# Performance work log

Hardware: AMD Instinct MI355X
Metric: run time of the kernel (lower is better)

Reference implementation:

```python
import jax, jax.numpy as jnp
import numpy as np
from jax import lax

STRIDE = 1
PAD = 1
KH = KW = 3


def conv2d(x, w, b=None, stride=STRIDE, pad=PAD):
    out = lax.conv_general_dilated(x, w, (stride, stride), [(pad, pad), (pad, pad)],
                                   dimension_numbers=("NCHW", "OIHW", "NCHW"))
    if b is not None:
        out = out + b[None, :, None, None]
    return out


def deform_conv2d(x, offset, mask, weight, stride=STRIDE, pad=PAD):
    """torchvision.ops.deform_conv2d (v2, single group) semantics."""
    B, C, H, W = x.shape
    Co, Ci, Kh, Kw = weight.shape
    K2 = Kh * Kw
    Ho = (H + 2 * pad - Kh) // stride + 1
    Wo = (W + 2 * pad - Kw) // stride + 1

    off = offset.reshape(B, K2, 2, Ho, Wo)  # [...,0]=dy, [...,1]=dx (row-major kernel order)
    ky = (jnp.arange(K2) // Kw).astype(x.dtype)
    kx = (jnp.arange(K2) % Kw).astype(x.dtype)
    hs = (jnp.arange(Ho) * stride - pad).astype(x.dtype)
    ws = (jnp.arange(Wo) * stride - pad).astype(x.dtype)

    # sampling coords [B, K2, Ho, Wo]
    py = off[:, :, 0] + hs[None, None, :, None] + ky[None, :, None, None]
    px = off[:, :, 1] + ws[None, None, None, :] + kx[None, :, None, None]

    y0 = jnp.floor(py)
    x0 = jnp.floor(px)
    wy1 = py - y0
    wx1 = px - x0
    wy0 = 1.0 - wy1
    wx0 = 1.0 - wx1
    y0i = y0.astype(jnp.int32)
    x0i = x0.astype(jnp.int32)

    xf = x.reshape(B, C, H * W)

    def gather(yi, xi):
        valid = (yi >= 0) & (yi < H) & (xi >= 0) & (xi < W)
        lin = jnp.clip(yi, 0, H - 1) * W + jnp.clip(xi, 0, W - 1)  # [B,K2,Ho,Wo]
        linf = lin.reshape(B, 1, -1)
        g = jnp.take_along_axis(xf, jnp.broadcast_to(linf, (B, C, linf.shape[-1])), axis=2)
        g = g.reshape(B, C, K2, Ho, Wo)
        return g * valid[:, None].astype(x.dtype)

    # bilinear combine, modulated by mask; v: [B, C, K2, Ho, Wo]
    v = ((wy0 * wx0)[:, None] * gather(y0i, x0i)
         + (wy0 * wx1)[:, None] * gather(y0i, x0i + 1)
         + (wy1 * wx0)[:, None] * gather(y0i + 1, x0i)
         + (wy1 * wx1)[:, None] * gather(y0i + 1, x0i + 1))
    v = v * mask[:, None]

    return jnp.einsum('bckhw,ock->bohw', v, weight.reshape(Co, Ci, K2))


def setup_inputs() -> dict:
    key = jax.random.key(0)
    ks = jax.random.split(key, 6)
    B, C, H, W = 2, 256, 64, 64
    Co = 256
    fan = C * KH * KW
    return {
        "x": jax.random.normal(ks[0], (B, C, H, W), jnp.float32),
        "residual": jax.random.normal(ks[1], (B, C, H, W), jnp.float32),
        "offset_w": jax.random.normal(ks[2], (2 * KH * KW, C, KH, KW), jnp.float32) * np.sqrt(2.0 / fan),
        "offset_b": jnp.zeros((2 * KH * KW,), jnp.float32),
        "mod_w": jax.random.normal(ks[3], (KH * KW, C, KH, KW), jnp.float32) * np.sqrt(2.0 / fan),
        "mod_b": jnp.zeros((KH * KW,), jnp.float32),
        "reg_w": jax.random.normal(ks[4], (Co, C, KH, KW), jnp.float32) * np.sqrt(2.0 / fan),
    }


def reference(x, residual, offset_w, offset_b, mod_w, mod_b, reg_w):
    offset = conv2d(residual, offset_w, offset_b)
    modulator = 2.0 * jax.nn.sigmoid(conv2d(x, mod_w, mod_b))
    return deform_conv2d(x, offset, modulator, reg_w)
```

## Files before the change

### kernel.cpp

```cpp
#include <hip/hip_runtime.h>
#include <hip/hip_bf16.h>
#include <math.h>

#define BB 2
#define CC 256
#define HH 64
#define WW 64
#define COo 256
#define HWs 4096
#define K2 9
#define CK 2304

typedef __attribute__((ext_vector_type(4))) float floatx4;
typedef __attribute__((ext_vector_type(8))) short shortx8;

#define O_OFF   0
#define O_MASK  147456
#define O_WBF   221184
#define O_WPK   516096
#define O_XT    10027008
#define O_RT    11075584

__device__ __forceinline__ void gll16(const __hip_bfloat16* g, __hip_bfloat16* l) {
    __builtin_amdgcn_global_load_lds(
        (const __attribute__((address_space(1))) unsigned int*)g,
        (__attribute__((address_space(3))) unsigned int*)l, 16, 0, 0);
}

__device__ __forceinline__ short f2bf(float v) {
    __hip_bfloat16 h = __float2bfloat16(v);
    return *reinterpret_cast<short*>(&h);
}

__device__ __forceinline__ float bf2f(short s) {
    unsigned u = ((unsigned)(unsigned short)s) << 16;
    return __builtin_bit_cast(float, u);
}

__global__ __launch_bounds__(256) void prep_kernel(
    const float* __restrict__ x,
    const float* __restrict__ residual,
    const float* __restrict__ reg_w,
    const float* __restrict__ off_w,
    const float* __restrict__ mod_w,
    __hip_bfloat16* __restrict__ xT,
    __hip_bfloat16* __restrict__ resT,
    __hip_bfloat16* __restrict__ Wbf,
    __hip_bfloat16* __restrict__ Wpk)
{
    int blk = blockIdx.x;
    int t = threadIdx.x;
    if (blk < 2048) {
        int sel = blk >> 10;
        int bk  = blk & 1023;
        int oc = bk & 7;
        int y  = (bk >> 3) & 63;
        int b  = bk >> 9;
        int wo = t & 63;
        int cg = t >> 6;
        int c0 = oc * 32 + cg * 8;
        const float* src = (sel ? residual : x)
                           + ((size_t)(b * CC + c0) * HH + y) * WW + wo;
        shortx8 pk;
#pragma unroll
        for (int j = 0; j < 8; ++j) pk[j] = f2bf(src[(size_t)j * HWs]);
        __hip_bfloat16* dst = sel ? resT : xT;
        *(shortx8*)(dst + ((size_t)b * 4096 + y * 64 + wo) * 256 + c0) = pk;
    } else {
        int idx = (blk - 2048) * 256 + t;
        if (idx < CK * COo) {
            int co = idx / CK;
            int r  = idx - co * CK;
            int k  = r >> 8;
            int c  = r & 255;
            Wbf[idx] = __float2bfloat16(reg_w[(size_t)co * CK + c * 9 + k]);
        }
        if (idx < 147456) {
            int g    = idx / 73728;
            int rem  = idx % 73728;
            int kc   = rem / 9216;
            int r2   = rem % 9216;
            int tap  = r2 / 1024;
            int r3   = r2 & 1023;
            int nf   = r3 >> 9;
            int r4   = r3 & 511;
            int lane = r4 >> 3;
            int j    = r4 & 7;
            int c    = kc * 32 + (lane >> 4) * 8 + j;
            int n    = nf * 16 + (lane & 15);
            float v = 0.f;
            if (g == 0) { if (n < 18) v = off_w[((size_t)n * CC + c) * 9 + tap]; }
            else        { if (n < 9)  v = mod_w[((size_t)n * CC + c) * 9 + tap]; }
            Wpk[idx] = __float2bfloat16(v);
        }
    }
}

__global__ __launch_bounds__(512) void convA2_kernel(
    const __hip_bfloat16* __restrict__ xT,
    const __hip_bfloat16* __restrict__ resT,
    const __hip_bfloat16* __restrict__ Wpk,
    const float* __restrict__ off_b,
    const float* __restrict__ mod_b,
    float* __restrict__ off_out,
    float* __restrict__ mask_out)
{
    int blk = blockIdx.x;
    int tile = blk & 127;
    int g = (blk >> 7) & 1;
    int b = blk >> 8;
    int t = threadIdx.x;
    int lane = t & 63;
    int w = t >> 6;
    int ph = w & 1;
    int ks = w >> 1;
    int ln = lane & 15;
    int quad = lane >> 4;

    const __hip_bfloat16* src = (g ? xT : resT) + (size_t)b * 4096 * 256;
    const __hip_bfloat16* wg  = Wpk + (size_t)g * 73728 + (size_t)ks * 2 * 9216;

    int pix = tile * 32 + ph * 16 + ln;
    int ho = pix >> 6, wo = pix & 63;

    floatx4 acc0 = (floatx4){0.f, 0.f, 0.f, 0.f};
    floatx4 acc1 = (floatx4){0.f, 0.f, 0.f, 0.f};

#pragma unroll
    for (int tap = 0; tap < 9; ++tap) {
        int ky = tap / 3, kx = tap % 3;
        int r  = ho + ky - 1;
        int cx = wo + kx - 1;
        bool v = (r >= 0) && (r < HH) && (cx >= 0) && (cx < WW);
        int hw = v ? (r * WW + cx) : 0;
        const __hip_bfloat16* abase = src + (size_t)hw * 256 + quad * 8 + ks * 64;
        const __hip_bfloat16* wbase = wg + (size_t)tap * 1024 + lane * 8;
#pragma unroll
        for (int kc = 0; kc < 2; ++kc) {
            shortx8 af = *(const shortx8*)(abase + kc * 32);
            if (!v) {
                shortx8 zf = {0,0,0,0,0,0,0,0};
                af = zf;
            }
            shortx8 b0 = *(const shortx8*)(wbase + (size_t)kc * 9216);
            shortx8 b1 = *(const shortx8*)(wbase + (size_t)kc * 9216 + 512);
            acc0 = __builtin_amdgcn_mfma_f32_16x16x32_bf16(af, b0, acc0, 0, 0, 0);
            acc1 = __builtin_amdgcn_mfma_f32_16x16x32_bf16(af, b1, acc1, 0, 0, 0);
        }
    }

    __shared__ float s_red[8][64][8];
    *(floatx4*)&s_red[w][lane][0] = acc0;
    *(floatx4*)&s_red[w][lane][4] = acc1;
    __syncthreads();
    if (w < 2) {
#pragma unroll
        for (int j = 0; j < 4; ++j) {
            acc0[j] = s_red[w][lane][j]     + s_red[w + 2][lane][j]
                    + s_red[w + 4][lane][j] + s_red[w + 6][lane][j];
            acc1[j] = s_red[w][lane][4 + j]     + s_red[w + 2][lane][4 + j]
                    + s_red[w + 4][lane][4 + j] + s_red[w + 6][lane][4 + j];
        }

#pragma unroll
        for (int nf = 0; nf < 2; ++nf) {
            floatx4 a = nf ? acc1 : acc0;
            int n = nf * 16 + ln;
#pragma unroll
            for (int i2 = 0; i2 < 4; ++i2) {
                int p = tile * 32 + w * 16 + quad * 4 + i2;
                if (g == 0) {
                    if (n < 18)
                        off_out[((size_t)b * 18 + n) * HWs + p] = a[i2] + off_b[n];
                } else {
                    if (n < 9) {
                        float z = a[i2] + mod_b[n];
                        mask_out[((size_t)b * 9 + n) * HWs + p] =
                            2.f / (1.f + __expf(-z));
                    }
                }
            }
        }
    }
}

__global__ __launch_bounds__(256) void gemm_fused_kernel(
    const __hip_bfloat16* __restrict__ xT,
    const float* __restrict__ off,
    const float* __restrict__ mask,
    const __hip_bfloat16* __restrict__ Wbf,
    float* __restrict__ out)
{
    int blk0 = blockIdx.x;
    int blk = ((blk0 & 7) << 6) | (blk0 >> 3);
    int nt = blk & 1;
    int mt = blk >> 1;
    int t  = threadIdx.x;
    int lane = t & 63;
    int w    = t >> 6;
    int quad = lane >> 4;
    int ln   = lane & 15;
    int wm = w & 1;
    int wn = w >> 1;

    __shared__ __hip_bfloat16 As[2][32 * 64];
    __shared__ __hip_bfloat16 Bs[2][128 * 64];
    __shared__ int   s_mi[32][K2][4];
    __shared__ float s_mw[32][K2][4];
    __shared__ float s_out[4][16 * 20];

    int b = mt >> 7;
    const __hip_bfloat16* xb = xT + (size_t)b * 4096 * 256;

    int lr8 = lane >> 3;
    int sub = lane & 7;
    int chk = sub ^ lr8;

    const __hip_bfloat16* gB = Wbf + (size_t)(nt * 128 + w * 8 + lr8) * CK + chk * 8;
    int lof = w * 512;

    floatx4 acc[4];
#pragma unroll
    for (int nf = 0; nf < 4; ++nf) acc[nf] = (floatx4){0.f, 0.f, 0.f, 0.f};

#pragma unroll
    for (int h = 0; h < 4; ++h)
        gll16(gB + (size_t)(h * 32) * CK, &Bs[0][lof + h * 2048]);

    for (int u = t; u < 32 * K2; u += 256) {
        int pl_ = u / K2;
        int k  = u - pl_ * K2;
        int pix = mt * 32 + pl_;
        int hw = pix & 4095;
        int ho = hw >> 6, wo = hw & 63;
        float dy = off [(((size_t)b * 18 + 2 * k    ) << 12) + hw];
        float dx = off [(((size_t)b * 18 + 2 * k + 1) << 12) + hw];
        float m  = mask[(((size_t)b * 9  + k        ) << 12) + hw];
        float py = (float)(ho - 1 + k / 3) + dy;
        float px = (float)(wo - 1 + k % 3) + dx;
        float y0f = floorf(py), x0f = floorf(px);
        float wy1 = py - y0f, wx1 = px - x0f;
        float wy0 = 1.f - wy1, wx0 = 1.f - wx1;
        int y0 = (int)y0f, x0 = (int)x0f;
#pragma unroll
        for (int j = 0; j < 4; ++j) {
            int yy = y0 + (j >> 1);
            int xx = x0 + (j & 1);
            float wj = ((j == 0) ? wy0 * wx0 :
                        (j == 1) ? wy0 * wx1 :
                        (j == 2) ? wy1 * wx0 : wy1 * wx1) * m;
            bool valid = (yy >= 0) && (yy < HH) && (xx >= 0) && (xx < WW);
            s_mi[pl_][k][j] = valid ? (yy * WW + xx) : 0;
            s_mw[pl_][k][j] = valid ? wj : 0.f;
        }
    }

    int pl  = t >> 3;
    int ch8 = t & 7;
    int aslot = pl * 64 + ((ch8 ^ (pl & 7)) * 8);

    int   mi0, mi1, mi2, mi3;
    float mw0, mw1, mw2, mw3;
    auto meta_load = [&](int k) {
        mi0 = s_mi[pl][k][0]; mi1 = s_mi[pl][k][1];
        mi2 = s_mi[pl][k][2]; mi3 = s_mi[pl][k][3];
        mw0 = s_mw[pl][k][0]; mw1 = s_mw[pl][k][1];
        mw2 = s_mw[pl][k][2]; mw3 = s_mw[pl][k][3];
    };

    shortx8 gc0, gc1, gc2, gc3;
    float   gw0, gw1, gw2, gw3;
    auto gather_load = [&](int cb) {
        const __hip_bfloat16* xr = xb + cb * 64 + ch8 * 8;
        gc0 = *(const shortx8*)(xr + (size_t)mi0 * 256);
        gc1 = *(const shortx8*)(xr + (size_t)mi1 * 256);
        gc2 = *(const shortx8*)(xr + (size_t)mi2 * 256);
        gc3 = *(const shortx8*)(xr + (size_t)mi3 * 256);
        gw0 = mw0; gw1 = mw1; gw2 = mw2; gw3 = mw3;
    };
    auto gather_store = [&](int buf) {
        shortx8 o;
#pragma unroll
        for (int j = 0; j < 8; ++j)
            o[j] = f2bf(gw0 * bf2f(gc0[j]) + gw1 * bf2f(gc1[j])
                      + gw2 * bf2f(gc2[j]) + gw3 * bf2f(gc3[j]));
        *(shortx8*)&As[buf][aslot] = o;
    };

    __syncthreads();
    meta_load(0);
    gather_load(0);
    gather_store(0);
    gather_load(1);

    int swz = ln & 7;

    for (int kt = 0; kt < 36; ++kt) {
        int cur = kt & 1;
        int nxt = cur ^ 1;
        __syncthreads();
        if (kt + 1 < 36) {
            int ko = (kt + 1) * 64;
#pragma unroll
            for (int h = 0; h < 4; ++h)
                gll16(gB + (size_t)(h * 32) * CK + ko, &Bs[nxt][lof + h * 2048]);
        }
#pragma unroll
        for (int kh = 0; kh < 2; ++kh) {
            int slot = ((kh * 4 + quad) ^ swz) * 8;
            shortx8 af = *(const shortx8*)
                &As[cur][(wm * 16 + ln) * 64 + slot];
            shortx8 bf[4];
#pragma unroll
            for (int nf = 0; nf < 4; ++nf)
                bf[nf] = *(const shortx8*)
                    &Bs[cur][(wn * 64 + nf * 16 + ln) * 64 + slot];
#pragma unroll
            for (int nf = 0; nf < 4; ++nf)
                acc[nf] = __builtin_amdgcn_mfma_f32_16x16x32_bf16(
                    af, bf[nf], acc[nf], 0, 0, 0);
        }
        if (kt + 1 < 36) gather_store(nxt);
        if (kt + 2 < 36) {
            int k2 = kt + 2;
            if ((k2 & 3) == 0) meta_load(k2 >> 2);
            gather_load(k2 & 3);
        }
    }

    int bb = mt >> 7;
    int hw0 = (mt & 127) * 32 + wm * 16;
    float* sw = &s_out[w][0];
    int co_l = lane >> 2;
    int seg  = lane & 3;
#pragma unroll
    for (int nf = 0; nf < 4; ++nf) {
        *(floatx4*)&sw[ln * 20 + quad * 4] = acc[nf];
        floatx4 v0 = *(const floatx4*)&sw[co_l * 20 + seg * 4];
        int co = nt * 128 + wn * 64 + nf * 16 + co_l;
        float* orow = out + ((size_t)(bb * COo + co) << 12) + hw0;
        *(floatx4*)&orow[seg * 4] = v0;
    }
}

extern "C" void kernel_launch(void* const* d_in, const int* in_sizes, int n_in,
                              void* d_out, int out_size, void* d_ws, size_t ws_size,
                              hipStream_t stream)
{
    const float* x     = (const float*)d_in[0];
    const float* resid = (const float*)d_in[1];
    const float* off_w = (const float*)d_in[2];
    const float* off_b = (const float*)d_in[3];
    const float* mod_w = (const float*)d_in[4];
    const float* mod_b = (const float*)d_in[5];
    const float* reg_w = (const float*)d_in[6];
    float* out = (float*)d_out;

    float* ws = (float*)d_ws;
    float* off_buf   = ws + O_OFF;
    float* mask_buf  = ws + O_MASK;
    __hip_bfloat16* Wbf  = (__hip_bfloat16*)(ws + O_WBF);
    __hip_bfloat16* Wpk  = (__hip_bfloat16*)(ws + O_WPK);
    __hip_bfloat16* xT   = (__hip_bfloat16*)(ws + O_XT);
    __hip_bfloat16* resT = (__hip_bfloat16*)(ws + O_RT);

    prep_kernel<<<2048 + (CK * COo + 255) / 256, 256, 0, stream>>>(
        x, resid, reg_w, off_w, mod_w, xT, resT, Wbf, Wpk);

    convA2_kernel<<<512, 512, 0, stream>>>(xT, resT, Wpk, off_b, mod_b,
                                           off_buf, mask_buf);

    gemm_fused_kernel<<<512, 256, 0, stream>>>(xT, off_buf, mask_buf, Wbf, out);
}
```

Baseline: 130.6 us.

## Fuse offset/mask convolution into deformable GEMM kernel via shared memory

Merges the offset and modulator 3x3 convolutions into the main deformable-conv GEMM kernel. Each block computes the offsets and masks for its 32 pixels with MFMA and keeps them in shared memory instead of writing them to and reading them from global buffers. This removes one kernel launch and the global round-trip. In exchange, both N-tile blocks recompute the same conv, and the per-block conv runs without split-K before the main loop, adding serial latency.

```diff
diff --git a/kernel.cpp b/kernel.cpp
--- a/kernel.cpp
+++ b/kernel.cpp
@@ -14,8 +14,6 @@
 typedef __attribute__((ext_vector_type(4))) float floatx4;
 typedef __attribute__((ext_vector_type(8))) short shortx8;
 
-#define O_OFF   0
-#define O_MASK  147456
 #define O_WBF   221184
 #define O_WPK   516096
 #define O_XT    10027008
@@ -96,98 +94,12 @@
     }
 }
 
-__global__ __launch_bounds__(512) void convA2_kernel(
+__global__ __launch_bounds__(256) void mega_kernel(
     const __hip_bfloat16* __restrict__ xT,
     const __hip_bfloat16* __restrict__ resT,
     const __hip_bfloat16* __restrict__ Wpk,
     const float* __restrict__ off_b,
     const float* __restrict__ mod_b,
-    float* __restrict__ off_out,
-    float* __restrict__ mask_out)
-{
-    int blk = blockIdx.x;
-    int tile = blk & 127;
-    int g = (blk >> 7) & 1;
-    int b = blk >> 8;
-    int t = threadIdx.x;
-    int lane = t & 63;
-    int w = t >> 6;
-    int ph = w & 1;
-    int ks = w >> 1;
-    int ln = lane & 15;
-    int quad = lane >> 4;
-
-    const __hip_bfloat16* src = (g ? xT : resT) + (size_t)b * 4096 * 256;
-    const __hip_bfloat16* wg  = Wpk + (size_t)g * 73728 + (size_t)ks * 2 * 9216;
-
-    int pix = tile * 32 + ph * 16 + ln;
-    int ho = pix >> 6, wo = pix & 63;
-
-    floatx4 acc0 = (floatx4){0.f, 0.f, 0.f, 0.f};
-    floatx4 acc1 = (floatx4){0.f, 0.f, 0.f, 0.f};
-
-#pragma unroll
-    for (int tap = 0; tap < 9; ++tap) {
-        int ky = tap / 3, kx = tap % 3;
-        int r  = ho + ky - 1;
-        int cx = wo + kx - 1;
-        bool v = (r >= 0) && (r < HH) && (cx >= 0) && (cx < WW);
-        int hw = v ? (r * WW + cx) : 0;
-        const __hip_bfloat16* abase = src + (size_t)hw * 256 + quad * 8 + ks * 64;
-        const __hip_bfloat16* wbase = wg + (size_t)tap * 1024 + lane * 8;
-#pragma unroll
-        for (int kc = 0; kc < 2; ++kc) {
-            shortx8 af = *(const shortx8*)(abase + kc * 32);
-            if (!v) {
-                shortx8 zf = {0,0,0,0,0,0,0,0};
-                af = zf;
-            }
-            shortx8 b0 = *(const shortx8*)(wbase + (size_t)kc * 9216);
-            shortx8 b1 = *(const shortx8*)(wbase + (size_t)kc * 9216 + 512);
-            acc0 = __builtin_amdgcn_mfma_f32_16x16x32_bf16(af, b0, acc0, 0, 0, 0);
-            acc1 = __builtin_amdgcn_mfma_f32_16x16x32_bf16(af, b1, acc1, 0, 0, 0);
-        }
-    }
-
-    __shared__ float s_red[8][64][8];
-    *(floatx4*)&s_red[w][lane][0] = acc0;
-    *(floatx4*)&s_red[w][lane][4] = acc1;
-    __syncthreads();
-    if (w < 2) {
-#pragma unroll
-        for (int j = 0; j < 4; ++j) {
-            acc0[j] = s_red[w][lane][j]     + s_red[w + 2][lane][j]
-                    + s_red[w + 4][lane][j] + s_red[w + 6][lane][j];
-            acc1[j] = s_red[w][lane][4 + j]     + s_red[w + 2][lane][4 + j]
-                    + s_red[w + 4][lane][4 + j] + s_red[w + 6][lane][4 + j];
-        }
-
-#pragma unroll
-        for (int nf = 0; nf < 2; ++nf) {
-            floatx4 a = nf ? acc1 : acc0;
-            int n = nf * 16 + ln;
-#pragma unroll
-            for (int i2 = 0; i2 < 4; ++i2) {
-                int p = tile * 32 + w * 16 + quad * 4 + i2;
-                if (g == 0) {
-                    if (n < 18)
-                        off_out[((size_t)b * 18 + n) * HWs + p] = a[i2] + off_b[n];
-                } else {
-                    if (n < 9) {
-                        float z = a[i2] + mod_b[n];
-                        mask_out[((size_t)b * 9 + n) * HWs + p] =
-                            2.f / (1.f + __expf(-z));
-                    }
-                }
-            }
-        }
-    }
-}
-
-__global__ __launch_bounds__(256) void gemm_fused_kernel(
-    const __hip_bfloat16* __restrict__ xT,
-    const float* __restrict__ off,
-    const float* __restrict__ mask,
     const __hip_bfloat16* __restrict__ Wbf,
     float* __restrict__ out)
 {
@@ -208,6 +120,8 @@
     __shared__ int   s_mi[32][K2][4];
     __shared__ float s_mw[32][K2][4];
     __shared__ float s_out[4][16 * 20];
+    __shared__ float s_off[32][18];
+    __shared__ float s_msk[32][9];
 
     int b = mt >> 7;
     const __hip_bfloat16* xb = xT + (size_t)b * 4096 * 256;
@@ -227,15 +141,70 @@
     for (int h = 0; h < 4; ++h)
         gll16(gB + (size_t)(h * 32) * CK, &Bs[0][lof + h * 2048]);
 
+    {
+        int cgv = w >> 1;
+        int cph = w & 1;
+        const __hip_bfloat16* csrc = (cgv ? xT : resT) + (size_t)b * 4096 * 256;
+        const __hip_bfloat16* cwg  = Wpk + (size_t)cgv * 73728;
+        int chwl = (mt & 127) * 32 + cph * 16 + ln;
+        int cho = chwl >> 6, cwo = chwl & 63;
+
+        floatx4 ca0 = (floatx4){0.f, 0.f, 0.f, 0.f};
+        floatx4 ca1 = (floatx4){0.f, 0.f, 0.f, 0.f};
+
+#pragma unroll
+        for (int tap = 0; tap < 9; ++tap) {
+            int ky = tap / 3, kx = tap % 3;
+            int r  = cho + ky - 1;
+            int cx = cwo + kx - 1;
+            bool v = (r >= 0) && (r < HH) && (cx >= 0) && (cx < WW);
+            int hw = v ? (r * WW + cx) : 0;
+            const __hip_bfloat16* abase = csrc + (size_t)hw * 256 + quad * 8;
+            const __hip_bfloat16* wbase = cwg + (size_t)tap * 1024 + lane * 8;
+#pragma unroll
+            for (int kc = 0; kc < 8; ++kc) {
+                shortx8 af = *(const shortx8*)(abase + kc * 32);
+                if (!v) {
+                    shortx8 zf = {0,0,0,0,0,0,0,0};
+                    af = zf;
+                }
+                shortx8 b0 = *(const shortx8*)(wbase + (size_t)kc * 9216);
+                ca0 = __builtin_amdgcn_mfma_f32_16x16x32_bf16(af, b0, ca0, 0, 0, 0);
+                if (cgv == 0) {
+                    shortx8 b1 = *(const shortx8*)(wbase + (size_t)kc * 9216 + 512);
+                    ca1 = __builtin_amdgcn_mfma_f32_16x16x32_bf16(af, b1, ca1, 0, 0, 0);
+                }
+            }
+        }
+
+        if (cgv == 0) {
+#pragma unroll
+            for (int i2 = 0; i2 < 4; ++i2) {
+                int p = cph * 16 + quad * 4 + i2;
+                s_off[p][ln] = ca0[i2] + off_b[ln];
+                if (ln < 2) s_off[p][16 + ln] = ca1[i2] + off_b[16 + ln];
+            }
+        } else {
+#pragma unroll
+            for (int i2 = 0; i2 < 4; ++i2) {
+                int p = cph * 16 + quad * 4 + i2;
+                if (ln < 9) {
+                    float z = ca0[i2] + mod_b[ln];
+                    s_msk[p][ln] = 2.f / (1.f + __expf(-z));
+                }
+            }
+        }
+    }
+    __syncthreads();
+
     for (int u = t; u < 32 * K2; u += 256) {
         int pl_ = u / K2;
         int k  = u - pl_ * K2;
-        int pix = mt * 32 + pl_;
-        int hw = pix & 4095;
+        int hw = (mt & 127) * 32 + pl_;
         int ho = hw >> 6, wo = hw & 63;
-        float dy = off [(((size_t)b * 18 + 2 * k    ) << 12) + hw];
-        float dx = off [(((size_t)b * 18 + 2 * k + 1) << 12) + hw];
-        float m  = mask[(((size_t)b * 9  + k        ) << 12) + hw];
+        float dy = s_off[pl_][2 * k];
+        float dx = s_off[pl_][2 * k + 1];
+        float m  = s_msk[pl_][k];
         float py = (float)(ho - 1 + k / 3) + dy;
         float px = (float)(wo - 1 + k % 3) + dx;
         float y0f = floorf(py), x0f = floorf(px);
@@ -357,8 +326,6 @@
     float* out = (float*)d_out;
 
     float* ws = (float*)d_ws;
-    float* off_buf   = ws + O_OFF;
-    float* mask_buf  = ws + O_MASK;
     __hip_bfloat16* Wbf  = (__hip_bfloat16*)(ws + O_WBF);
     __hip_bfloat16* Wpk  = (__hip_bfloat16*)(ws + O_WPK);
     __hip_bfloat16* xT   = (__hip_bfloat16*)(ws + O_XT);
@@ -367,8 +334,5 @@
     prep_kernel<<<2048 + (CK * COo + 255) / 256, 256, 0, stream>>>(
         x, resid, reg_w, off_w, mod_w, xT, resT, Wbf, Wpk);
 
-    convA2_kernel<<<512, 512, 0, stream>>>(xT, resT, Wpk, off_b, mod_b,
-                                           off_buf, mask_buf);
-
-    gemm_fused_kernel<<<512, 256, 0, stream>>>(xT, off_buf, mask_buf, Wbf, out);
-}
+    mega_kernel<<<512, 256, 0, stream>>>(xT, resT, Wpk, off_b, mod_b, Wbf, out);
+}
```

New measurement: 158.7 us. 1.22x slower.
